# Performance work log

Measured on AMD Instinct MI355X. Metric: run time of the kernel, lower is better.

## Reference

```python
import jax, jax.numpy as jnp
import numpy as np

B, S, D, H = 2, 4096, 512, 8


def setup_inputs() -> dict:
    key = jax.random.key(0)
    ks = jax.random.split(key, 8)
    sc = 1.0 / np.sqrt(D)
    return {
        "query": jax.random.normal(ks[0], (B, S, D), jnp.float32),
        "key_in": jax.random.normal(ks[1], (B, S, D), jnp.float32),
        "value": jax.random.normal(ks[2], (B, S, D), jnp.float32),
        "mask": jax.random.randint(ks[3], (B, S), 0, 2, jnp.int32),
        "Wq": jax.random.normal(ks[4], (D, D), jnp.float32) * sc,
        "bq": jnp.zeros((D,), jnp.float32),
        "Wk": jax.random.normal(ks[5], (D, D), jnp.float32) * sc,
        "bk": jnp.zeros((D,), jnp.float32),
        "Wv": jax.random.normal(ks[6], (D, D), jnp.float32) * sc,
        "bv": jnp.zeros((D,), jnp.float32),
        "Wo": jax.random.normal(ks[7], (D, D), jnp.float32) * sc,
        "bo": jnp.zeros((D,), jnp.float32),
    }


def reference(query, key_in, value, mask, Wq, bq, Wk, bk, Wv, bv, Wo, bo):
    b, s, d = query.shape
    dh = d // H  # per-head dim = out_size // attn_heads
    # projections + split heads: [B,S,D] -> [B,H,S,dh]
    q = (query @ Wq + bq).reshape(b, s, H, dh).transpose(0, 2, 1, 3)
    k = (key_in @ Wk + bk).reshape(b, s, H, dh).transpose(0, 2, 1, 3)
    v = (value @ Wv + bv).reshape(b, s, H, dh).transpose(0, 2, 1, 3)
    # scores / sqrt(dh); torch divides by sqrt(query.size(-1)) AFTER head split
    scores = jnp.einsum("bhqd,bhkd->bhqk", q, k) / jnp.sqrt(jnp.asarray(dh, q.dtype))
    # 2D mask broadcast: mask[:,None,None,:] == unsqueeze(1).repeat(1,S,1).unsqueeze(1)
    scores = jnp.where(mask[:, None, None, :] == 0, jnp.asarray(-1e9, scores.dtype), scores)
    p_attn = jax.nn.softmax(scores, axis=-1)  # dropout p=0.0 -> identity
    x = jnp.einsum("bhqk,bhkd->bhqd", p_attn, v)
    x = x.transpose(0, 2, 1, 3).reshape(b, s, H * dh)
    return x @ Wo + bo
```

## Files before the change

### kernel.cpp

```cpp
#include <hip/hip_runtime.h>
#include <math.h>

#define BATCH  2
#define SLEN   4096
#define DMODEL 512
#define NH     8
#define DH     64
#define NROWS  (BATCH * SLEN)

#define QSCALE 0.18033688011112042f
#define MBIAS  -65504.0f

typedef __attribute__((ext_vector_type(8)))  _Float16 f16x8;
typedef __attribute__((ext_vector_type(4)))  _Float16 f16x4;
typedef __attribute__((ext_vector_type(4)))  float    f32x4;
typedef __attribute__((ext_vector_type(16))) float    f32x16;
typedef __attribute__((ext_vector_type(4)))  unsigned int u32x4;

__device__ __forceinline__ float exp2_hw(float x) {
    float r; asm("v_exp_f32 %0, %1" : "=v"(r) : "v"(x)); return r;
}

__device__ __forceinline__ void pswap(unsigned &a, unsigned &b) {
    asm volatile("v_permlane32_swap_b32 %0, %1" : "+v"(a), "+v"(b));
}

__device__ __forceinline__ unsigned pkrtz(float a, float b) {
    auto p = __builtin_amdgcn_cvt_pkrtz(a, b);
    return __builtin_bit_cast(unsigned, p);
}

__device__ __forceinline__ void gload16(const void* g, void* l) {
    __builtin_amdgcn_global_load_lds(
        (const __attribute__((address_space(1))) unsigned int*)g,
        (__attribute__((address_space(3))) unsigned int*)l, 16, 0, 0);
}

__global__ __launch_bounds__(256)
void cast_weights(const float* __restrict__ W0, const float* __restrict__ W1,
                  const float* __restrict__ W2, const float* __restrict__ W3,
                  _Float16* __restrict__ T0, _Float16* __restrict__ T1,
                  _Float16* __restrict__ T2, _Float16* __restrict__ T3)
{
    const int z = blockIdx.z;
    const float* W = (z == 0) ? W0 : (z == 1) ? W1 : (z == 2) ? W2 : W3;
    _Float16*    T = (z == 0) ? T0 : (z == 1) ? T1 : (z == 2) ? T2 : T3;
    const float sc = (z == 0) ? QSCALE : 1.0f;

    __shared__ float Ls[32][33];
    const int n0 = blockIdx.x * 32, k0 = blockIdx.y * 32;
    const int row = threadIdx.x >> 3;
    const int c4  = (threadIdx.x & 7) << 2;

    float4 v = *(const float4*)&W[(size_t)(k0 + row) * DMODEL + n0 + c4];
    Ls[row][c4 + 0] = v.x; Ls[row][c4 + 1] = v.y;
    Ls[row][c4 + 2] = v.z; Ls[row][c4 + 3] = v.w;
    __syncthreads();

    f16x4 o;
    #pragma unroll
    for (int j = 0; j < 4; ++j) o[j] = (_Float16)(Ls[c4 + j][row] * sc);
    *(f16x4*)&T[(size_t)(n0 + row) * DMODEL + k0 + c4] = o;
}

template<int AMODE, int OUTMODE>
__global__ __launch_bounds__(256)
void gemm_mfma(const void* __restrict__ Ag, const _Float16* __restrict__ WTg,
               const float* __restrict__ bias, float bscale, void* __restrict__ Cout)
{
    extern __shared__ char smem[];
    char* Asb = smem;
    char* Bsb = smem + 8192;
    _Float16* Tr = (_Float16*)(smem + 16384);

    const int tid  = threadIdx.x;
    const int lane = tid & 63;
    const int w    = tid >> 6;
    const int g    = lane >> 4;
    const int c    = lane & 15;
    const int m0   = blockIdx.y * 64;
    const int n0   = blockIdx.x * 64;

    const int lrow = lane >> 3;
    const int schk = (lane & 7) ^ lrow;
    const int brow = w * 8 + lrow;
    const _Float16* bSrc0 = WTg + (size_t)(n0 + brow) * DMODEL + schk * 8;
    const _Float16* bSrc1 = WTg + (size_t)(n0 + brow + 32) * DMODEL + schk * 8;
    char* bDst = Bsb + w * 1024;
    char* aDst = Asb + w * 1024;

    const _Float16* aSrc0 = nullptr; const _Float16* aSrc1 = nullptr;
    const float* aF = nullptr;
    const int arow = tid >> 2;
    const int acp  = (tid & 3) << 1;
    if constexpr (AMODE == 0) {
        const _Float16* Ah = (const _Float16*)Ag;
        aSrc0 = Ah + (size_t)(m0 + brow) * DMODEL + schk * 8;
        aSrc1 = Ah + (size_t)(m0 + brow + 32) * DMODEL + schk * 8;
    } else {
        aF = (const float*)Ag + (size_t)(m0 + arow) * DMODEL;
    }

    f32x4 acc[4];
    #pragma unroll
    for (int nt = 0; nt < 4; ++nt) acc[nt] = (f32x4){0.f, 0.f, 0.f, 0.f};

    for (int k0 = 0; k0 < DMODEL; k0 += 64) {
        float4 a0, a1, a2, a3;
        if constexpr (AMODE == 1) {
            const float* p = aF + k0 + acp * 8;
            a0 = *(const float4*)(p + 0);  a1 = *(const float4*)(p + 4);
            a2 = *(const float4*)(p + 8);  a3 = *(const float4*)(p + 12);
        }
        __syncthreads();
        if constexpr (AMODE == 0) {
            gload16(aSrc0 + k0, aDst);
            gload16(aSrc1 + k0, aDst + 4096);
        } else {
            f16x8 h0, h1;
            h0[0]=(_Float16)a0.x; h0[1]=(_Float16)a0.y; h0[2]=(_Float16)a0.z; h0[3]=(_Float16)a0.w;
            h0[4]=(_Float16)a1.x; h0[5]=(_Float16)a1.y; h0[6]=(_Float16)a1.z; h0[7]=(_Float16)a1.w;
            h1[0]=(_Float16)a2.x; h1[1]=(_Float16)a2.y; h1[2]=(_Float16)a2.z; h1[3]=(_Float16)a2.w;
            h1[4]=(_Float16)a3.x; h1[5]=(_Float16)a3.y; h1[6]=(_Float16)a3.z; h1[7]=(_Float16)a3.w;
            *(f16x8*)(Asb + arow * 128 + (((acp    ) ^ (arow & 7)) << 4)) = h0;
            *(f16x8*)(Asb + arow * 128 + (((acp + 1) ^ (arow & 7)) << 4)) = h1;
        }
        gload16(bSrc0 + k0, bDst);
        gload16(bSrc1 + k0, bDst + 4096);
        __syncthreads();

        #pragma unroll
        for (int ks = 0; ks < 2; ++ks) {
            const int ar = w * 16 + c;
            f16x8 af = *(const f16x8*)(Asb + ar * 128 + ((((ks << 2) + g) ^ (ar & 7)) << 4));
            #pragma unroll
            for (int nt = 0; nt < 4; ++nt) {
                const int br = nt * 16 + c;
                f16x8 bf = *(const f16x8*)(Bsb + br * 128 + ((((ks << 2) + g) ^ (br & 7)) << 4));
                acc[nt] = __builtin_amdgcn_mfma_f32_16x16x32_f16(af, bf, acc[nt], 0, 0, 0);
            }
        }
    }

    const int h = n0 >> 6;
    if constexpr (OUTMODE == 0) {
        float* C = (float*)Cout;
        #pragma unroll
        for (int nt = 0; nt < 4; ++nt) {
            const float bb = bias[n0 + nt * 16 + c];
            #pragma unroll
            for (int r = 0; r < 4; ++r) {
                const int m = m0 + w * 16 + g * 4 + r;
                C[(size_t)m * DMODEL + n0 + nt * 16 + c] = acc[nt][r] + bb;
            }
        }
    } else if constexpr (OUTMODE == 1) {
        _Float16* C = (_Float16*)Cout;
        #pragma unroll
        for (int nt = 0; nt < 4; ++nt) {
            const float bb = bias[n0 + nt * 16 + c] * bscale;
            const int hd = nt * 16 + c;
            #pragma unroll
            for (int r = 0; r < 4; ++r) {
                const int m = m0 + w * 16 + g * 4 + r;
                const int b = m >> 12;
                const int s = m & (SLEN - 1);
                C[(((size_t)b * NH + h) * SLEN + s) * DH + hd] = (_Float16)(acc[nt][r] + bb);
            }
        }
    } else {
        #pragma unroll
        for (int nt = 0; nt < 4; ++nt) {
            const float bb = bias[n0 + nt * 16 + c];
            #pragma unroll
            for (int r = 0; r < 4; ++r)
                Tr[(size_t)(w * 64 + nt * 16 + c) * 24 + g * 4 + r] = (_Float16)(acc[nt][r] + bb);
        }
        const int n = lane;
        f16x8 t0 = *(const f16x8*)&Tr[(size_t)(w * 64 + n) * 24 + 0];
        f16x8 t1 = *(const f16x8*)&Tr[(size_t)(w * 64 + n) * 24 + 8];
        const int b = m0 >> 12;
        const int s = (m0 & (SLEN - 1)) + w * 16;
        _Float16* dst = (_Float16*)Cout + (((size_t)b * NH + h) * DH + n) * SLEN + s;
        *(f16x8*)dst = t0;
        *(f16x8*)(dst + 8) = t1;
    }
}

__global__ __launch_bounds__(256, 2)
void flash_mfma32(const _Float16* __restrict__ Qg, const _Float16* __restrict__ Kg,
                  const _Float16* __restrict__ Vtg, const int* __restrict__ mask,
                  _Float16* __restrict__ X)
{
    __shared__ char KsB[8192];
    __shared__ char VsB[8192];
    __shared__ _Float16 Mb[64];
    __shared__ _Float16 Osc[4][32][72];

    const int tid  = threadIdx.x;
    const int lane = tid & 63;
    const int w    = tid >> 6;
    const int q    = lane & 31;
    const int h    = lane >> 5;

    const int wg  = blockIdx.x;
    const int ii  = wg >> 3;
    const int bh  = (wg & 7) * 2 + (ii >> 5);
    const int qt  = ii & 31;
    const int b   = bh >> 3;
    const int hh  = bh & 7;
    const int q0  = qt * 128;

    const _Float16* Kb  = Kg  + (size_t)bh * SLEN * DH;
    const _Float16* Vtb = Vtg + (size_t)bh * DH * SLEN;
    const int* mrow = mask + (size_t)b * SLEN;

    const _Float16* Qb = Qg + ((size_t)bh * SLEN + q0 + w * 32 + q) * DH;
    f16x8 qf[4];
    #pragma unroll
    for (int ds = 0; ds < 4; ++ds) qf[ds] = *(const f16x8*)(Qb + ds * 16 + h * 8);

    f16x8 ef = (f16x8)(_Float16)0;
    if (h == 0) ef[0] = (_Float16)1;
    f16x8 onesA;
    #pragma unroll
    for (int i = 0; i < 8; ++i) onesA[i] = (_Float16)1;

    const int l8   = lane >> 3;
    const int schk = (lane & 7) ^ l8;
    const _Float16* kS0 = Kb  + (size_t)(w * 8 + l8) * DH + schk * 8;
    const _Float16* kS1 = kS0 + (size_t)32 * DH;
    const _Float16* vS0 = Vtb + (size_t)(w * 8 + l8) * SLEN + schk * 8;
    const _Float16* vS1 = vS0 + (size_t)32 * SLEN;
    char* kD0 = KsB + w * 1024;  char* kD1 = KsB + 4096 + w * 1024;
    char* vD0 = VsB + w * 1024;  char* vD1 = VsB + 4096 + w * 1024;

    float  mrun = -INFINITY;
    f32x16 lacc = (f32x16)0.f;
    f32x16 oacc[2];
    oacc[0] = (f32x16)0.f; oacc[1] = (f32x16)0.f;

    for (int kt = 0; kt < SLEN / 64; ++kt) {
        const int k0 = kt << 6;
        __syncthreads();
        gload16(kS0 + (size_t)k0 * DH, kD0);
        gload16(kS1 + (size_t)k0 * DH, kD1);
        gload16(vS0 + k0, vD0);
        gload16(vS1 + k0, vD1);
        if (tid < 64) Mb[tid] = mrow[k0 + tid] ? (_Float16)0 : (_Float16)MBIAS;
        __syncthreads();

        f32x16 st[2];
        #pragma unroll
        for (int kt2 = 0; kt2 < 2; ++kt2) {
            f16x8 mf = (f16x8)(_Float16)0;
            if (h == 0) mf[0] = Mb[q + kt2 * 32];
            st[kt2] = __builtin_amdgcn_mfma_f32_32x32x16_f16(mf, ef, (f32x16)0.f, 0, 0, 0);
            #pragma unroll
            for (int ds = 0; ds < 4; ++ds) {
                const int row = kt2 * 32 + q;
                f16x8 kf = *(const f16x8*)(KsB + row * 128 + ((((ds << 1) + h) ^ (row & 7)) << 4));
                st[kt2] = __builtin_amdgcn_mfma_f32_32x32x16_f16(kf, qf[ds], st[kt2], 0, 0, 0);
            }
        }

        float a[16];
        #pragma unroll
        for (int e = 0; e < 16; ++e) a[e] = fmaxf(st[0][e], st[1][e]);
        #pragma unroll
        for (int s2 = 8; s2 >= 1; s2 >>= 1) {
            #pragma unroll
            for (int e = 0; e < 8; ++e)
                if (e < s2) a[e] = fmaxf(a[e], a[e + s2]);
        }
        float mx = fmaxf(a[0], __shfl_xor(a[0], 32));
        const float mn   = fmaxf(mrun, mx);
        const float corr = exp2_hw(mrun - mn);
        mrun = mn;

        #pragma unroll
        for (int kt2 = 0; kt2 < 2; ++kt2) {
            #pragma unroll
            for (int e = 0; e < 16; ++e)
                st[kt2][e] = exp2_hw(st[kt2][e] - mn);
        }
        lacc[0] *= corr;
        #pragma unroll
        for (int e = 0; e < 16; ++e) { oacc[0][e] *= corr; oacc[1][e] *= corr; }

        #pragma unroll
        for (int ks = 0; ks < 4; ++ks) {
            const int kt2 = ks >> 1, bs = (ks & 1) * 8;
            unsigned W0 = pkrtz(st[kt2][bs + 0], st[kt2][bs + 1]);
            unsigned W1 = pkrtz(st[kt2][bs + 2], st[kt2][bs + 3]);
            unsigned W2 = pkrtz(st[kt2][bs + 4], st[kt2][bs + 5]);
            unsigned W3 = pkrtz(st[kt2][bs + 6], st[kt2][bs + 7]);
            pswap(W0, W2);
            pswap(W1, W3);
            u32x4 pw; pw[0] = W0; pw[1] = W1; pw[2] = W2; pw[3] = W3;
            f16x8 pb = __builtin_bit_cast(f16x8, pw);

            lacc = __builtin_amdgcn_mfma_f32_32x32x16_f16(onesA, pb, lacc, 0, 0, 0);
            #pragma unroll
            for (int dt = 0; dt < 2; ++dt) {
                const int row = dt * 32 + q;
                f16x8 vf = *(const f16x8*)(VsB + row * 128 + ((((ks << 1) + h) ^ (row & 7)) << 4));
                oacc[dt] = __builtin_amdgcn_mfma_f32_32x32x16_f16(vf, pb, oacc[dt], 0, 0, 0);
            }
        }
    }

    const float inv = 1.0f / lacc[0];
    #pragma unroll
    for (int dt = 0; dt < 2; ++dt) {
        #pragma unroll
        for (int r = 0; r < 16; r += 2) {
            const int d = dt * 32 + (r & 3) + 8 * (r >> 2) + 4 * h;
            *(unsigned*)&Osc[w][q][d] = pkrtz(oacc[dt][r] * inv, oacc[dt][r + 1] * inv);
        }
    }
    const int qr  = lane >> 1;
    const int dh2 = (lane & 1) * 32;
    _Float16* dst = X + ((size_t)b * SLEN + q0 + w * 32 + qr) * DMODEL + hh * DH + dh2;
    #pragma unroll
    for (int p = 0; p < 4; ++p)
        *(f16x8*)(dst + p * 8) = *(const f16x8*)&Osc[w][qr][dh2 + p * 8];
}

extern "C" void kernel_launch(void* const* d_in, const int* in_sizes, int n_in,
                              void* d_out, int out_size, void* d_ws, size_t ws_size,
                              hipStream_t stream)
{
    const float* query  = (const float*)d_in[0];
    const float* key_in = (const float*)d_in[1];
    const float* value  = (const float*)d_in[2];
    const int*   mask   = (const int*)  d_in[3];
    const float* Wq = (const float*)d_in[4];
    const float* bq = (const float*)d_in[5];
    const float* Wk = (const float*)d_in[6];
    const float* bk = (const float*)d_in[7];
    const float* Wv = (const float*)d_in[8];
    const float* bv = (const float*)d_in[9];
    const float* Wo = (const float*)d_in[10];
    const float* bo = (const float*)d_in[11];
    float* out = (float*)d_out;
    (void)in_sizes; (void)n_in; (void)out_size; (void)ws_size;

    const size_t NE = (size_t)NROWS * DMODEL;
    const size_t WN = (size_t)DMODEL * DMODEL;
    _Float16* f   = (_Float16*)d_ws;
    _Float16* qh  = f;
    _Float16* kh  = f + NE;
    _Float16* vth = f + 2 * NE;
    _Float16* xh  = f + 3 * NE;
    _Float16* wqT = f + 4 * NE;
    _Float16* wkT = wqT + WN;
    _Float16* wvT = wkT + WN;
    _Float16* woT = wvT + WN;

    cast_weights<<<dim3(16, 16, 4), 256, 0, stream>>>(Wq, Wk, Wv, Wo, wqT, wkT, wvT, woT);

    dim3 gg(DMODEL / 64, NROWS / 64);
    gemm_mfma<1, 1><<<gg, 256, 16384, stream>>>(query,  wqT, bq, QSCALE, qh);
    gemm_mfma<1, 1><<<gg, 256, 16384, stream>>>(key_in, wkT, bk, 1.0f,   kh);
    gemm_mfma<1, 2><<<gg, 256, 28672, stream>>>(value,  wvT, bv, 1.0f,   vth);

    flash_mfma32<<<512, 256, 0, stream>>>(qh, kh, vth, mask, xh);

    gemm_mfma<0, 0><<<gg, 256, 16384, stream>>>(xh, woT, bo, 1.0f, out);
}
```

Measured before the change: 195.6 us.

## Double-buffer K/V tiles in flash kernel, premask, lazy rescale, raise occupancy

The flash-attention loop now double-buffers the K/V shared-memory tiles. The next tile's global-to-LDS loads are issued before computing on the current one, which removes one barrier per iteration. The mask is converted to an fp16 bias in a separate small kernel and read straight into registers instead of being staged through LDS. Online-softmax rescaling is skipped unless the running max grows by more than a threshold, and MFMA sections are given raised wave priority. Launch bounds ask for 4 blocks per CU, which may force register spills, and the lazy rescale relies on fp32 headroom to stay accurate.

```diff
diff --git a/kernel.cpp b/kernel.cpp
--- a/kernel.cpp
+++ b/kernel.cpp
@@ -61,6 +61,13 @@
     #pragma unroll
     for (int j = 0; j < 4; ++j) o[j] = (_Float16)(Ls[c4 + j][row] * sc);
     *(f16x4*)&T[(size_t)(n0 + row) * DMODEL + k0 + c4] = o;
+}
+
+__global__ __launch_bounds__(256)
+void cast_mask(const int* __restrict__ mask, _Float16* __restrict__ mb)
+{
+    const int i = blockIdx.x * 256 + threadIdx.x;
+    mb[i] = mask[i] ? (_Float16)0.0f : (_Float16)MBIAS;
 }
 
 template<int AMODE, int OUTMODE>
@@ -187,15 +194,12 @@
     }
 }
 
-__global__ __launch_bounds__(256, 2)
+__global__ __launch_bounds__(256, 4)
 void flash_mfma32(const _Float16* __restrict__ Qg, const _Float16* __restrict__ Kg,
-                  const _Float16* __restrict__ Vtg, const int* __restrict__ mask,
+                  const _Float16* __restrict__ Vtg, const _Float16* __restrict__ mb16,
                   _Float16* __restrict__ X)
 {
-    __shared__ char KsB[8192];
-    __shared__ char VsB[8192];
-    __shared__ _Float16 Mb[64];
-    __shared__ _Float16 Osc[4][32][72];
+    __shared__ char SB[32768];
 
     const int tid  = threadIdx.x;
     const int lane = tid & 63;
@@ -213,7 +217,7 @@
 
     const _Float16* Kb  = Kg  + (size_t)bh * SLEN * DH;
     const _Float16* Vtb = Vtg + (size_t)bh * DH * SLEN;
-    const int* mrow = mask + (size_t)b * SLEN;
+    const _Float16* mbrow = mb16 + (size_t)b * SLEN;
 
     const _Float16* Qb = Qg + ((size_t)bh * SLEN + q0 + w * 32 + q) * DH;
     f16x8 qf[4];
@@ -232,29 +236,44 @@
     const _Float16* kS1 = kS0 + (size_t)32 * DH;
     const _Float16* vS0 = Vtb + (size_t)(w * 8 + l8) * SLEN + schk * 8;
     const _Float16* vS1 = vS0 + (size_t)32 * SLEN;
-    char* kD0 = KsB + w * 1024;  char* kD1 = KsB + 4096 + w * 1024;
-    char* vD0 = VsB + w * 1024;  char* vD1 = VsB + 4096 + w * 1024;
 
     float  mrun = -INFINITY;
     f32x16 lacc = (f32x16)0.f;
     f32x16 oacc[2];
     oacc[0] = (f32x16)0.f; oacc[1] = (f32x16)0.f;
 
+    {
+        char* d = SB + w * 1024;
+        gload16(kS0, d);
+        gload16(kS1, d + 4096);
+        gload16(vS0, d + 8192);
+        gload16(vS1, d + 12288);
+    }
+    _Float16 mn0 = mbrow[q], mn1 = mbrow[32 + q];
+
+    int cur = 0;
     for (int kt = 0; kt < SLEN / 64; ++kt) {
-        const int k0 = kt << 6;
         __syncthreads();
-        gload16(kS0 + (size_t)k0 * DH, kD0);
-        gload16(kS1 + (size_t)k0 * DH, kD1);
-        gload16(vS0 + k0, vD0);
-        gload16(vS1 + k0, vD1);
-        if (tid < 64) Mb[tid] = mrow[k0 + tid] ? (_Float16)0 : (_Float16)MBIAS;
-        __syncthreads();
+        const _Float16 mc0 = mn0, mc1 = mn1;
+        if (kt + 1 < SLEN / 64) {
+            const int k0n = (kt + 1) << 6;
+            char* d = SB + ((cur ^ 1) << 14) + w * 1024;
+            gload16(kS0 + (size_t)k0n * DH, d);
+            gload16(kS1 + (size_t)k0n * DH, d + 4096);
+            gload16(vS0 + k0n, d + 8192);
+            gload16(vS1 + k0n, d + 12288);
+            mn0 = mbrow[k0n + q];
+            mn1 = mbrow[k0n + 32 + q];
+        }
+        const char* KsB = SB + (cur << 14);
+        const char* VsB = KsB + 8192;
 
         f32x16 st[2];
+        __builtin_amdgcn_s_setprio(1);
         #pragma unroll
         for (int kt2 = 0; kt2 < 2; ++kt2) {
             f16x8 mf = (f16x8)(_Float16)0;
-            if (h == 0) mf[0] = Mb[q + kt2 * 32];
+            if (h == 0) mf[0] = kt2 ? mc1 : mc0;
             st[kt2] = __builtin_amdgcn_mfma_f32_32x32x16_f16(mf, ef, (f32x16)0.f, 0, 0, 0);
             #pragma unroll
             for (int ds = 0; ds < 4; ++ds) {
@@ -263,6 +282,7 @@
                 st[kt2] = __builtin_amdgcn_mfma_f32_32x32x16_f16(kf, qf[ds], st[kt2], 0, 0, 0);
             }
         }
+        __builtin_amdgcn_s_setprio(0);
 
         float a[16];
         #pragma unroll
@@ -273,21 +293,25 @@
             for (int e = 0; e < 8; ++e)
                 if (e < s2) a[e] = fmaxf(a[e], a[e + s2]);
         }
-        float mx = fmaxf(a[0], __shfl_xor(a[0], 32));
-        const float mn   = fmaxf(mrun, mx);
-        const float corr = exp2_hw(mrun - mn);
-        mrun = mn;
+        const float mx = fmaxf(a[0], __shfl_xor(a[0], 32));
+
+        if (!__all(mx <= mrun + 8.0f)) {
+            const float mn = fmaxf(mrun, mx);
+            const float corr = exp2_hw(mrun - mn);
+            mrun = mn;
+            lacc[0] *= corr;
+            #pragma unroll
+            for (int e = 0; e < 16; ++e) { oacc[0][e] *= corr; oacc[1][e] *= corr; }
+        }
 
         #pragma unroll
         for (int kt2 = 0; kt2 < 2; ++kt2) {
             #pragma unroll
             for (int e = 0; e < 16; ++e)
-                st[kt2][e] = exp2_hw(st[kt2][e] - mn);
-        }
-        lacc[0] *= corr;
-        #pragma unroll
-        for (int e = 0; e < 16; ++e) { oacc[0][e] *= corr; oacc[1][e] *= corr; }
-
+                st[kt2][e] = exp2_hw(st[kt2][e] - mrun);
+        }
+
+        __builtin_amdgcn_s_setprio(1);
         #pragma unroll
         for (int ks = 0; ks < 4; ++ks) {
             const int kt2 = ks >> 1, bs = (ks & 1) * 8;
@@ -308,15 +332,20 @@
                 oacc[dt] = __builtin_amdgcn_mfma_f32_32x32x16_f16(vf, pb, oacc[dt], 0, 0, 0);
             }
         }
-    }
-
+        __builtin_amdgcn_s_setprio(0);
+        cur ^= 1;
+    }
+
+    __syncthreads();
+    _Float16* Osc = (_Float16*)SB;
     const float inv = 1.0f / lacc[0];
     #pragma unroll
     for (int dt = 0; dt < 2; ++dt) {
         #pragma unroll
         for (int r = 0; r < 16; r += 2) {
             const int d = dt * 32 + (r & 3) + 8 * (r >> 2) + 4 * h;
-            *(unsigned*)&Osc[w][q][d] = pkrtz(oacc[dt][r] * inv, oacc[dt][r + 1] * inv);
+            *(unsigned*)&Osc[(w * 32 + q) * 72 + d] =
+                pkrtz(oacc[dt][r] * inv, oacc[dt][r + 1] * inv);
         }
     }
     const int qr  = lane >> 1;
@@ -324,7 +353,7 @@
     _Float16* dst = X + ((size_t)b * SLEN + q0 + w * 32 + qr) * DMODEL + hh * DH + dh2;
     #pragma unroll
     for (int p = 0; p < 4; ++p)
-        *(f16x8*)(dst + p * 8) = *(const f16x8*)&Osc[w][qr][dh2 + p * 8];
+        *(f16x8*)(dst + p * 8) = *(const f16x8*)&Osc[(w * 32 + qr) * 72 + dh2 + p * 8];
 }
 
 extern "C" void kernel_launch(void* const* d_in, const int* in_sizes, int n_in,
@@ -357,15 +386,17 @@
     _Float16* wkT = wqT + WN;
     _Float16* wvT = wkT + WN;
     _Float16* woT = wvT + WN;
+    _Float16* mb16 = woT + WN;
 
     cast_weights<<<dim3(16, 16, 4), 256, 0, stream>>>(Wq, Wk, Wv, Wo, wqT, wkT, wvT, woT);
+    cast_mask<<<NROWS / 256, 256, 0, stream>>>(mask, mb16);
 
     dim3 gg(DMODEL / 64, NROWS / 64);
     gemm_mfma<1, 1><<<gg, 256, 16384, stream>>>(query,  wqT, bq, QSCALE, qh);
     gemm_mfma<1, 1><<<gg, 256, 16384, stream>>>(key_in, wkT, bk, 1.0f,   kh);
     gemm_mfma<1, 2><<<gg, 256, 28672, stream>>>(value,  wvT, bv, 1.0f,   vth);
 
-    flash_mfma32<<<512, 256, 0, stream>>>(qh, kh, vth, mask, xh);
+    flash_mfma32<<<512, 256, 0, stream>>>(qh, kh, vth, mb16, xh);
 
     gemm_mfma<0, 0><<<gg, 256, 16384, stream>>>(xh, woT, bo, 1.0f, out);
 }
```

Result: slower. 215.9 us (+10.4%).

## Split attention over two key halves and merge partial softmax results

Applied to the files above, without the earlier changes.

The flash attention kernel now splits the key sequence into two halves, so the grid doubles from 512 to 1024 workgroups. Each workgroup writes a normalized partial output plus its running max and sum. A new combine kernel then merges the two halves with log-sum-exp weights into the head-interleaved X buffer. The aim is better occupancy across the 256 CUs, since 512 workgroups cover them only once or twice. The cost is an extra kernel launch, extra global traffic for the fp16 partials, and a tighter launch bound of 4 that may pressure registers.

```diff
diff --git a/kernel.cpp b/kernel.cpp
--- a/kernel.cpp
+++ b/kernel.cpp
@@ -7,6 +7,8 @@
 #define NH     8
 #define DH     64
 #define NROWS  (BATCH * SLEN)
+#define NSPLIT 2
+#define KSPLIT (SLEN / NSPLIT)
 
 #define QSCALE 0.18033688011112042f
 #define MBIAS  -65504.0f
@@ -187,10 +189,10 @@
     }
 }
 
-__global__ __launch_bounds__(256, 2)
-void flash_mfma32(const _Float16* __restrict__ Qg, const _Float16* __restrict__ Kg,
-                  const _Float16* __restrict__ Vtg, const int* __restrict__ mask,
-                  _Float16* __restrict__ X)
+__global__ __launch_bounds__(256, 4)
+void flash_split(const _Float16* __restrict__ Qg, const _Float16* __restrict__ Kg,
+                 const _Float16* __restrict__ Vtg, const int* __restrict__ mask,
+                 _Float16* __restrict__ Op, float2* __restrict__ ML)
 {
     __shared__ char KsB[8192];
     __shared__ char VsB[8192];
@@ -203,17 +205,20 @@
     const int q    = lane & 31;
     const int h    = lane >> 5;
 
-    const int wg  = blockIdx.x;
-    const int ii  = wg >> 3;
-    const int bh  = (wg & 7) * 2 + (ii >> 5);
-    const int qt  = ii & 31;
-    const int b   = bh >> 3;
-    const int hh  = bh & 7;
-    const int q0  = qt * 128;
+    const int wg    = blockIdx.x;
+    const int xcd   = wg & 7;
+    const int idx   = wg >> 3;
+    const int combo = xcd * 4 + (idx >> 5);
+    const int qt    = idx & 31;
+    const int bh    = combo >> 1;
+    const int sp    = combo & 1;
+    const int b     = bh >> 3;
+    const int q0    = qt * 128;
+    const int kbase = sp * KSPLIT;
 
     const _Float16* Kb  = Kg  + (size_t)bh * SLEN * DH;
     const _Float16* Vtb = Vtg + (size_t)bh * DH * SLEN;
-    const int* mrow = mask + (size_t)b * SLEN;
+    const int* mrow = mask + (size_t)b * SLEN + kbase;
 
     const _Float16* Qb = Qg + ((size_t)bh * SLEN + q0 + w * 32 + q) * DH;
     f16x8 qf[4];
@@ -228,9 +233,9 @@
 
     const int l8   = lane >> 3;
     const int schk = (lane & 7) ^ l8;
-    const _Float16* kS0 = Kb  + (size_t)(w * 8 + l8) * DH + schk * 8;
+    const _Float16* kS0 = Kb  + (size_t)(kbase + w * 8 + l8) * DH + schk * 8;
     const _Float16* kS1 = kS0 + (size_t)32 * DH;
-    const _Float16* vS0 = Vtb + (size_t)(w * 8 + l8) * SLEN + schk * 8;
+    const _Float16* vS0 = Vtb + (size_t)(w * 8 + l8) * SLEN + kbase + schk * 8;
     const _Float16* vS1 = vS0 + (size_t)32 * SLEN;
     char* kD0 = KsB + w * 1024;  char* kD1 = KsB + 4096 + w * 1024;
     char* vD0 = VsB + w * 1024;  char* vD1 = VsB + 4096 + w * 1024;
@@ -240,7 +245,7 @@
     f32x16 oacc[2];
     oacc[0] = (f32x16)0.f; oacc[1] = (f32x16)0.f;
 
-    for (int kt = 0; kt < SLEN / 64; ++kt) {
+    for (int kt = 0; kt < KSPLIT / 64; ++kt) {
         const int k0 = kt << 6;
         __syncthreads();
         gload16(kS0 + (size_t)k0 * DH, kD0);
@@ -319,12 +324,46 @@
             *(unsigned*)&Osc[w][q][d] = pkrtz(oacc[dt][r] * inv, oacc[dt][r + 1] * inv);
         }
     }
+    const size_t qabs = (size_t)(sp * 16 + bh) * SLEN + q0 + w * 32;
+    if (h == 0) ML[qabs + q] = make_float2(mrun, lacc[0]);
+
     const int qr  = lane >> 1;
     const int dh2 = (lane & 1) * 32;
-    _Float16* dst = X + ((size_t)b * SLEN + q0 + w * 32 + qr) * DMODEL + hh * DH + dh2;
+    _Float16* dst = Op + (qabs + qr) * DH + dh2;
     #pragma unroll
     for (int p = 0; p < 4; ++p)
         *(f16x8*)(dst + p * 8) = *(const f16x8*)&Osc[w][qr][dh2 + p * 8];
+}
+
+__global__ __launch_bounds__(256)
+void combine_split(const _Float16* __restrict__ Op, const float2* __restrict__ ML,
+                   _Float16* __restrict__ X)
+{
+    const int bh = blockIdx.x >> 7;
+    const int qb = blockIdx.x & 127;
+    const int q  = qb * 32 + (threadIdx.x >> 3);
+    const int dc = (threadIdx.x & 7) * 8;
+
+    const size_t i1 = (size_t)bh * SLEN + q;
+    const size_t i2 = (size_t)(16 + bh) * SLEN + q;
+    const float2 ml1 = ML[i1];
+    const float2 ml2 = ML[i2];
+    const float m  = fmaxf(ml1.x, ml2.x);
+    const float a1 = exp2_hw(ml1.x - m) * ml1.y;
+    const float a2 = exp2_hw(ml2.x - m) * ml2.y;
+    const float w1 = a1 / (a1 + a2);
+    const float w2 = 1.0f - w1;
+
+    f16x8 o1 = *(const f16x8*)(Op + i1 * DH + dc);
+    f16x8 o2 = *(const f16x8*)(Op + i2 * DH + dc);
+    f16x8 o;
+    #pragma unroll
+    for (int j = 0; j < 8; ++j)
+        o[j] = (_Float16)(w1 * (float)o1[j] + w2 * (float)o2[j]);
+
+    const int b  = bh >> 3;
+    const int hh = bh & 7;
+    *(f16x8*)(X + ((size_t)b * SLEN + q) * DMODEL + hh * DH + dc) = o;
 }
 
 extern "C" void kernel_launch(void* const* d_in, const int* in_sizes, int n_in,
@@ -348,6 +387,7 @@
 
     const size_t NE = (size_t)NROWS * DMODEL;
     const size_t WN = (size_t)DMODEL * DMODEL;
+    const size_t OPN = (size_t)NSPLIT * NH * BATCH * SLEN * DH;
     _Float16* f   = (_Float16*)d_ws;
     _Float16* qh  = f;
     _Float16* kh  = f + NE;
@@ -357,6 +397,8 @@
     _Float16* wkT = wqT + WN;
     _Float16* wvT = wkT + WN;
     _Float16* woT = wvT + WN;
+    _Float16* opart = woT + WN;
+    float2*   mlpart = (float2*)(opart + OPN);
 
     cast_weights<<<dim3(16, 16, 4), 256, 0, stream>>>(Wq, Wk, Wv, Wo, wqT, wkT, wvT, woT);
 
@@ -365,7 +407,8 @@
     gemm_mfma<1, 1><<<gg, 256, 16384, stream>>>(key_in, wkT, bk, 1.0f,   kh);
     gemm_mfma<1, 2><<<gg, 256, 28672, stream>>>(value,  wvT, bv, 1.0f,   vth);
 
-    flash_mfma32<<<512, 256, 0, stream>>>(qh, kh, vth, mask, xh);
+    flash_split<<<1024, 256, 0, stream>>>(qh, kh, vth, mask, opart, mlpart);
+    combine_split<<<2048, 256, 0, stream>>>(opart, mlpart, xh);
 
     gemm_mfma<0, 0><<<gg, 256, 16384, stream>>>(xh, woT, bo, 1.0f, out);
 }
```

Result: slower. 200.1 us (+2.3%).
